# Performance work log

Measured on AMD Instinct MI355X. Metric: run time of the kernel, lower is better.

Reference implementation:

```python
import jax, jax.numpy as jnp
import numpy as np

B, S, T = 64, 1024, 64
H, A, DA, DT, P, NT = 1024, 1024, 512, 256, 256, 32
DIN = DA + A + DT  # LSTMCell input: [a_tm1_embed, att_tm1, pre_type]


def setup_inputs() -> dict:
    key = jax.random.key(0)
    ks = jax.random.split(key, 16)
    nrm = lambda k, shape, s=0.02: jax.random.normal(k, shape, jnp.float32) * s
    return {
        'src_encodings': jax.random.normal(ks[0], (B, S, H), jnp.float32),
        'W_ih': nrm(ks[1], (4 * H, DIN)), 'b_ih': jnp.zeros((4 * H,), jnp.float32),
        'W_hh': nrm(ks[2], (4 * H, H)), 'b_hh': jnp.zeros((4 * H,), jnp.float32),
        'W_att': nrm(ks[3], (H, H)),            # att_sketch_linear (no bias)
        'W_attvec': nrm(ks[4], (A, 2 * H)),     # sketch_att_vec_linear (no bias)
        'W_init': nrm(ks[5], (H, H)), 'b_init': jnp.zeros((H,), jnp.float32),  # decoder_cell_init
        'W_q2a': nrm(ks[6], (DA, A)), 'b_q2a': jnp.zeros((DA,), jnp.float32),  # query_vec_to_action_embed
        'prod_embed': nrm(ks[7], (P, DA), 0.05), 'prod_bias': jnp.zeros((P,), jnp.float32),
        'type_embed': nrm(ks[8], (NT, DT), 0.05),
        'prev_prod_ids': jax.random.randint(ks[9], (B, T), 0, P),
        'prev_type_ids': jax.random.randint(ks[10], (B, T), 0, NT),
        'target_prod_ids': jax.random.randint(ks[11], (B, T), 0, P),
        'sketch_lens': jax.random.randint(ks[12], (B,), T // 2, T + 1),
        'src_lens': jax.random.randint(ks[13], (B,), S // 2, S + 1),
    }


def _lstm_cell(x, h, c, W_ih, b_ih, W_hh, b_hh):
    gates = x @ W_ih.T + b_ih + h @ W_hh.T + b_hh
    i, f, g, o = jnp.split(gates, 4, axis=-1)
    c_new = jax.nn.sigmoid(f) * c + jax.nn.sigmoid(i) * jnp.tanh(g)
    h_new = jax.nn.sigmoid(o) * jnp.tanh(c_new)
    return h_new, c_new


def reference(src_encodings, W_ih, b_ih, W_hh, b_hh, W_att, W_attvec, W_init, b_init,
              W_q2a, b_q2a, prod_embed, prod_bias, type_embed,
              prev_prod_ids, prev_type_ids, target_prod_ids, sketch_lens, src_lens):
    Bq, Sq, Hq = src_encodings.shape
    Tq = prev_prod_ids.shape[1]
    src_valid = jnp.arange(Sq)[None, :] < src_lens[:, None]            # [B,S] True = real token
    step_valid = jnp.arange(Tq)[None, :] < sketch_lens[:, None]        # [B,T]
    prev_valid = step_valid & (jnp.arange(Tq)[None, :] > 0)            # prev action exists

    src_att = jnp.einsum('bsh,kh->bsk', src_encodings, W_att)          # att_sketch_linear
    # init_decoder_state(adaptive_avg_pool1d(enc,1))
    init_cell = src_encodings.mean(axis=1)
    h0 = jnp.tanh(init_cell @ W_init.T + b_init)
    c0 = jnp.zeros_like(h0)
    att0 = jnp.zeros((Bq, A), src_encodings.dtype)

    # precomputed grammar lookups (production / type embeddings of a_{t-1})
    a_embeds = jnp.where(prev_valid[..., None], prod_embed[prev_prod_ids], 0.0)   # [B,T,DA]
    t_embeds = jnp.where(prev_valid[..., None], type_embed[prev_type_ids], 0.0)   # [B,T,DT]
    is_first = jnp.arange(Tq) == 0                                                # [T]

    def step(carry, inp):
        h, c, att_tm1 = carry
        a_e, t_e, first = inp
        x = jnp.concatenate([a_e, att_tm1, t_e], axis=-1)
        x = jnp.where(first, 0.0, x)                                   # t==0 -> zero input
        h, c = _lstm_cell(x, h, c, W_ih, b_ih, W_hh, b_hh)
        scores = jnp.einsum('bh,bsh->bs', h, src_att)
        scores = jnp.where(src_valid, scores, -1e9)
        alpha = jax.nn.softmax(scores, axis=-1)
        ctx = jnp.einsum('bs,bsh->bh', alpha, src_encodings)
        att_t = jnp.tanh(jnp.concatenate([h, ctx], axis=-1) @ W_attvec.T)
        q = jnp.tanh(att_t @ W_q2a.T + b_q2a)                          # non_linear readout
        probs = jax.nn.softmax(q @ prod_embed.T + prod_bias, axis=-1)  # [B,P]
        return (h, c, att_t), probs

    xs = (jnp.swapaxes(a_embeds, 0, 1), jnp.swapaxes(t_embeds, 0, 1), is_first)
    _, probs = jax.lax.scan(step, (h0, c0, att0), xs)                  # [T,B,P]

    tgt = jnp.swapaxes(target_prod_ids, 0, 1)[..., None]               # [T,B,1]
    p_t = jnp.take_along_axis(probs, tgt, axis=-1)[..., 0]             # [T,B]
    logp = jnp.log(p_t + 1e-8)
    sketch_prob = jnp.sum(jnp.where(step_valid.T, logp, 0.0), axis=0)  # [B]
    return sketch_prob
```

## Files before the change

### kernel.cpp

```cpp
#include <hip/hip_runtime.h>
#include <hip/hip_bf16.h>

typedef unsigned short u16;
typedef unsigned char u8;
typedef unsigned int u32;
typedef unsigned long long u64;
typedef __attribute__((ext_vector_type(8))) short short8;
typedef __attribute__((ext_vector_type(8))) u16 ushort8;
typedef __attribute__((ext_vector_type(4))) float f32x4;
typedef __attribute__((ext_vector_type(2))) float f32x2;

__device__ __forceinline__ float bf2f(u16 x){ u32 u=((u32)x)<<16; return __builtin_bit_cast(float,u); }
__device__ __forceinline__ u16 f2bf(float f){ u32 u=__builtin_bit_cast(u32,f); u32 r=(u+0x7fffu+((u>>16)&1u))>>16; return (u16)r; }
__device__ __forceinline__ float sigf(float x){ return 1.f/(1.f+__expf(-x)); }

__device__ __forceinline__ void scf(float* p, float v){
  __hip_atomic_store(p, v, __ATOMIC_RELAXED, __HIP_MEMORY_SCOPE_AGENT);
}
__device__ __forceinline__ void scu16(u16* p, u16 v){
  __hip_atomic_store(p, v, __ATOMIC_RELAXED, __HIP_MEMORY_SCOPE_AGENT);
}


__global__ __launch_bounds__(256) void k_cast(const float* __restrict__ s, u16* __restrict__ d, long n){
  long i = ((long)blockIdx.x*256 + threadIdx.x)*8;
  if (i >= n) return;
  float4 a = *(const float4*)(s+i);
  float4 b = *(const float4*)(s+i+4);
  ushort8 o;
  o[0]=f2bf(a.x); o[1]=f2bf(a.y); o[2]=f2bf(a.z); o[3]=f2bf(a.w);
  o[4]=f2bf(b.x); o[5]=f2bf(b.y); o[6]=f2bf(b.z); o[7]=f2bf(b.w);
  *(ushort8*)(d+i) = o;
}

__global__ __launch_bounds__(256) void k_cast8(const float* __restrict__ s, u8* __restrict__ d, long n){
  long i = ((long)blockIdx.x*256 + threadIdx.x)*8;
  if (i >= n) return;
  float4 a = *(const float4*)(s+i);
  float4 b = *(const float4*)(s+i+4);
  u32 w0 = 0, w1 = 0;
  w0 = __builtin_amdgcn_cvt_pk_fp8_f32(a.x, a.y, w0, false);
  w0 = __builtin_amdgcn_cvt_pk_fp8_f32(a.z, a.w, w0, true);
  w1 = __builtin_amdgcn_cvt_pk_fp8_f32(b.x, b.y, w1, false);
  w1 = __builtin_amdgcn_cvt_pk_fp8_f32(b.z, b.w, w1, true);
  uint2 o; o.x = w0; o.y = w1;
  *(uint2*)(d+i) = o;
}

__global__ __launch_bounds__(256) void k_build_wc(const float* __restrict__ Wih, const float* __restrict__ Whh,
                                                  u16* __restrict__ WC){
  long i8 = (long)blockIdx.x*256 + threadIdx.x;
  if (i8 >= (long)4096*352) return;
  int j = (int)(i8/352); int kk = (int)(i8%352)*8;
  const float* src;
  if (kk < 512)        src = Wih + (long)j*1792 + kk;
  else if (kk < 768)   src = Wih + (long)j*1792 + (kk+1024);
  else if (kk < 1792)  src = Wih + (long)j*1792 + (kk-256);
  else                 src = Whh + (long)j*1024 + (kk-1792);
  u16* dst = WC + (long)j*2816 + kk;
  ushort8 o;
  #pragma unroll
  for (int q=0;q<8;++q) o[q] = f2bf(src[q]);
  *(ushort8*)dst = o;
}

__global__ __launch_bounds__(256) void k_wattT(const float* __restrict__ Wa, u16* __restrict__ WT){
  int id = blockIdx.x*256 + threadIdx.x;
  int m = id >> 10, k = id & 1023;
  WT[(long)m*1024 + k] = f2bf(Wa[(long)k*1024 + m]);
}

__global__ __launch_bounds__(256) void k_meanf(const float* __restrict__ enc, u16* __restrict__ MEANB){
  int b = blockIdx.x, h = blockIdx.y*256 + threadIdx.x;
  const float* p = enc + ((long)b<<20) + h;
  float s = 0.f;
  for (int ss=0; ss<1024; ++ss) s += p[(long)ss<<10];
  MEANB[b*1024 + h] = f2bf(s * (1.f/1024.f));
}

__global__ __launch_bounds__(256) void k_embed(const float* __restrict__ pemb, const float* __restrict__ temb,
      const int* __restrict__ pid, const int* __restrict__ tid_, const int* __restrict__ slen,
      u16* __restrict__ XC){
  int t = blockIdx.x >> 6, b = blockIdx.x & 63;
  bool valid = (t>0) && (t < slen[b]);
  int pi = pid[b*64 + t], ti = tid_[b*64 + t];
  u16* dst = XC + (long)blockIdx.x*2816;
  for (int kk = threadIdx.x; kk < 768; kk += 256){
    float v = 0.f;
    if (valid) v = (kk<512) ? pemb[(long)pi*512 + kk] : temb[(long)ti*256 + (kk-512)];
    dst[kk] = f2bf(v);
  }
}

__global__ void k_assign(const int* __restrict__ slen, int* __restrict__ ASG){
  if (threadIdx.x != 0 || blockIdx.x != 0) return;
  int lenv[64]; long total = 0;
  for (int b=0;b<64;++b){ int L = slen[b]; if (L<1)L=1; if (L>1024)L=1024; lenv[b]=L; total+=L; }
  int cnt[64]; int sum=0;
  for (int b=0;b<64;++b){
    int c = (int)(((long)256*lenv[b])/total);
    if (c<1)c=1; if (c>8)c=8; cnt[b]=c; sum+=c;
  }
  int rem = 256 - sum; int bi = 0;
  while (rem > 0){ if (cnt[bi&63] < 8){ cnt[bi&63]++; rem--; } bi++; }
  while (rem < 0){ if (cnt[bi&63] > 1){ cnt[bi&63]--; rem++; } bi++; }
  int st = 0;
  for (int b=0;b<64;++b){
    ASG[1024+b] = cnt[b];
    ASG[1088+b] = st;
    for (int i=0;i<cnt[b];++i){ ASG[st+i] = b; ASG[256+st+i] = i; }
    st += cnt[b];
  }
}

template<int MODE>
__global__ __launch_bounds__(256) void k_gemm(const u16* __restrict__ A, long lda,
      const u16* __restrict__ W, int K, const float* __restrict__ bias,
      float* __restrict__ OF, long ldo, u16* __restrict__ OB1, long ldb1){
  int l = threadIdx.x & 63, w = threadIdx.x >> 6;
  int c = l & 15, g = l >> 4;
  int n0 = blockIdx.x*16, m0 = blockIdx.y*64;
  const u16* ap = A + (long)(m0 + w*16 + c)*lda + g*8;
  const u16* bp = W + (long)(n0 + c)*K + g*8;
  f32x4 acc = {0.f,0.f,0.f,0.f};
  int kit = K >> 5;
  #pragma unroll 4
  for (int kb=0; kb<kit; ++kb){
    short8 av = *(const short8*)(ap + kb*32);
    short8 bv = *(const short8*)(bp + kb*32);
    acc = __builtin_amdgcn_mfma_f32_16x16x32_bf16(av, bv, acc, 0, 0, 0);
  }
  #pragma unroll
  for (int r=0;r<4;++r){
    int row = m0 + w*16 + g*4 + r;
    int col = n0 + c;
    float v = acc[r];
    if (MODE==2){ OB1[(long)row*ldb1 + col] = f2bf(tanhf(v + bias[col])); }
    if (MODE==3){ OF[(long)row*ldo + col] = v + bias[col]; }
  }
}

__global__ __launch_bounds__(256) void k_loss(const float* __restrict__ LG, const int* __restrict__ tgt,
      const int* __restrict__ slen, float* __restrict__ out){
  int b = blockIdx.x;
  int w = threadIdx.x >> 6, l = threadIdx.x & 63;
  int len = slen[b];
  float accum = 0.f;
  for (int t = w; t < 64; t += 4){
    if (t >= len) continue;
    const float* lp = LG + ((long)(t*64 + b))*256;
    float v0=lp[l], v1=lp[l+64], v2=lp[l+128], v3=lp[l+192];
    float mx = fmaxf(fmaxf(v0,v1), fmaxf(v2,v3));
    #pragma unroll
    for (int off=32; off; off>>=1) mx = fmaxf(mx, __shfl_xor(mx, off));
    float s = __expf(v0-mx)+__expf(v1-mx)+__expf(v2-mx)+__expf(v3-mx);
    #pragma unroll
    for (int off=32; off; off>>=1) s += __shfl_xor(s, off);
    float ltg = lp[tgt[b*64 + t]];
    float p = __expf(ltg - mx)/s;
    accum += logf(p + 1e-8f);
  }
  __shared__ float sm[4];
  if (l == 0) sm[w] = accum;
  __syncthreads();
  if (threadIdx.x == 0) out[b] = sm[0]+sm[1]+sm[2]+sm[3];
}

__device__ __forceinline__ void gsync(int* __restrict__ bar, int& gen){
  gen += 1;
  __syncthreads();
  if (threadIdx.x == 0){
    int grp = blockIdx.x & 15;
    int prev = __hip_atomic_fetch_add(bar + grp*64, 1, __ATOMIC_RELAXED, __HIP_MEMORY_SCOPE_AGENT);
    if (prev == gen*16 - 1)
      __hip_atomic_fetch_add(bar + 1024, 1, __ATOMIC_RELAXED, __HIP_MEMORY_SCOPE_AGENT);
    while (__hip_atomic_load(bar + 1024, __ATOMIC_RELAXED, __HIP_MEMORY_SCOPE_AGENT) < gen*16)
      __builtin_amdgcn_s_sleep(1);
  }
  __syncthreads();
}

__global__ __launch_bounds__(1024,1) void k_decoder(
      const u8* __restrict__ ENC8, const u16* __restrict__ WC,
      const u16* __restrict__ WAVT, const u16* __restrict__ WAVEC,
      const float* __restrict__ bih, const float* __restrict__ bhh,
      u16* __restrict__ XC, u16* __restrict__ ATT,
      float* __restrict__ HWT, float* __restrict__ PLT,
      u16* __restrict__ CTXBT, const int* __restrict__ src_lens,
      const int* __restrict__ ASG, int* __restrict__ BAR){
  const int tid = threadIdx.x;
  const int w = tid >> 6, l = tid & 63, c = l & 15, g = l >> 4;
  const int bx = blockIdx.x;
  int gen = 0;

  __shared__ float smem[12320];
  f32x4* lacc  = (f32x4*)smem;
  float* s_ctx = smem;
  float* s_ls  = smem + 12288;
  u16*   ldsc  = (u16*)smem;
  f32x4* lacc4 = (f32x4*)(smem + 8192);

  const int n0 = bx << 2;
  const int jrow = n0 + (c & 3) + ((c >> 2) << 10);
  const float biasj = bih[jrow] + bhh[jrow];
  const int kh = w >> 2, mt = w & 3;
  const int lbase = l & 0x33;
  float creg[4] = {0.f,0.f,0.f,0.f};
  const int mt2 = bx & 3, nt2 = bx >> 2;
  const int b3 = ASG[bx];
  const int ci3 = ASG[256 + bx];
  const int nch3 = ASG[1024 + b3];
  int len3 = src_lens[b3]; if (len3 < 1) len3 = 1; if (len3 > 1024) len3 = 1024;
  const int chunk3 = (len3 + nch3 - 1)/nch3;
  int s0 = ci3*chunk3;
  int s1 = s0 + chunk3; if (s1 > len3) s1 = len3; if (s0 > s1) s0 = s1;
  const u8* encb = ENC8 + (((long)b3)<<20);
  const int base = s0 + 2*w;
  const int mt4 = bx & 3, nt4 = bx >> 2;
  const int b16 = tid >> 6, lane64 = tid & 63;

  uint4 pa0,pa1, pb0,pb1;
  {
    int rA0 = (base   < s1) ? base   : s0;
    int rA1 = (base+1 < s1) ? base+1 : s0;
    pa0 = *(const uint4*)(encb + ((long)rA0<<10) + l*16);
    pa1 = *(const uint4*)(encb + ((long)rA1<<10) + l*16);
    int sB = base+32;
    int rB0 = (sB   < s1) ? sB   : s0;
    int rB1 = (sB+1 < s1) ? sB+1 : s0;
    pb0 = *(const uint4*)(encb + ((long)rB0<<10) + l*16);
    pb1 = *(const uint4*)(encb + ((long)rB1<<10) + l*16);
  }

  for (int t = 0; t < 64; ++t){
    const u16* XCt = XC + (size_t)t*64*2816;
    u16* XCn = XC + (size_t)(t+1)*64*2816;
    const u16* Hcur = XCn + 1792;
    float* HW   = HWT  + ((size_t)t<<16);
    float* PL   = PLT  + ((size_t)t<<8);
    u16*  CTXB  = CTXBT + ((size_t)t<<18);

    {
      const u16* ap = XCt + (long)(mt*16 + c)*2816 + kh*704 + g*8;
      const u16* bp = WC  + (long)jrow*2816 + kh*704 + g*8;
      f32x4 acc = {0.f,0.f,0.f,0.f};
      #pragma unroll 11
      for (int kb=0; kb<22; ++kb){
        short8 av = *(const short8*)(ap + kb*32);
        short8 bv = *(const short8*)(bp + kb*32);
        acc = __builtin_amdgcn_mfma_f32_16x16x32_bf16(av, bv, acc, 0, 0, 0);
      }
      lacc[w*64 + l] = acc;
      __syncthreads();
      if (w < 4){
        f32x4 a0 = lacc[w*64 + l];
        f32x4 a1 = lacc[(w+4)*64 + l];
        f32x4 a2 = lacc[(w+8)*64 + l];
        f32x4 a3 = lacc[(w+12)*64 + l];
        #pragma unroll
        for (int r=0;r<4;++r){
          float val = a0[r] + a1[r] + a2[r] + a3[r] + biasj;
          float iv = __shfl(val, lbase);
          float fv = __shfl(val, lbase+4);
          float gv = __shfl(val, lbase+8);
          float ov = __shfl(val, lbase+12);
          if ((l & 12) == 0){
            float cn = sigf(fv)*creg[r] + sigf(iv)*tanhf(gv);
            float hn = sigf(ov)*tanhf(cn);
            creg[r] = cn;
            int b = w*16 + g*4 + r;
            int n = n0 + (l & 3);
            scu16(XCn + (long)b*2816 + 1792 + n, f2bf(hn));
          }
        }
      }
    }
    gsync(BAR, gen);

    {
      const u16* ap = Hcur + (long)(mt2*16 + c)*2816 + w*64 + g*8;
      const u16* bp = WAVT + (long)(nt2*16 + c)*1024 + w*64 + g*8;
      f32x4 acc = {0.f,0.f,0.f,0.f};
      #pragma unroll
      for (int kb=0; kb<2; ++kb){
        short8 av = *(const short8*)(ap + kb*32);
        short8 bv = *(const short8*)(bp + kb*32);
        acc = __builtin_amdgcn_mfma_f32_16x16x32_bf16(av, bv, acc, 0, 0, 0);
      }
      lacc[w*64 + l] = acc;
      __syncthreads();
      if (w == 0){
        f32x4 rd = lacc[l];
        #pragma unroll
        for (int w2=1; w2<16; ++w2) rd += lacc[w2*64 + l];
        #pragma unroll
        for (int r=0;r<4;++r)
          scf(HW + (long)(mt2*16 + g*4 + r)*1024 + nt2*16 + c, rd[r]);
      }
    }
    gsync(BAR, gen);

    {
      float hw[16], ctx[16];
      const float* hwp = HW + b3*1024 + l*16;
      #pragma unroll
      for (int jj=0;jj<4;++jj){
        float4 v = *(const float4*)(hwp + jj*4);
        hw[4*jj]=v.x; hw[4*jj+1]=v.y; hw[4*jj+2]=v.z; hw[4*jj+3]=v.w;
      }
      #pragma unroll
      for (int jj=0;jj<16;++jj) ctx[jj]=0.f;
      float lsum = 0.f;
      for (int s = base; s < s1; s += 32){
        int sC = s + 64;
        int rC0 = (sC   < s1) ? sC   : s0;
        int rC1 = (sC+1 < s1) ? sC+1 : s0;
        uint4 pc0 = *(const uint4*)(encb + ((long)rC0<<10) + l*16);
        uint4 pc1 = *(const uint4*)(encb + ((long)rC1<<10) + l*16);
        float eA[16], eB[16];
        #pragma unroll
        for (int jj=0;jj<4;++jj){
          u32 xA = ((const u32*)&pa0)[jj];
          u32 xB = ((const u32*)&pa1)[jj];
          f32x2 la = __builtin_amdgcn_cvt_pk_f32_fp8(xA, false);
          f32x2 ha = __builtin_amdgcn_cvt_pk_f32_fp8(xA, true);
          f32x2 lb = __builtin_amdgcn_cvt_pk_f32_fp8(xB, false);
          f32x2 hb = __builtin_amdgcn_cvt_pk_f32_fp8(xB, true);
          eA[4*jj]=la[0]; eA[4*jj+1]=la[1]; eA[4*jj+2]=ha[0]; eA[4*jj+3]=ha[1];
          eB[4*jj]=lb[0]; eB[4*jj+1]=lb[1]; eB[4*jj+2]=hb[0]; eB[4*jj+3]=hb[1];
        }
        float scA = 0.f, scB = 0.f;
        #pragma unroll
        for (int jj=0;jj<16;++jj){ scA += eA[jj]*hw[jj]; scB += eB[jj]*hw[jj]; }
        #pragma unroll
        for (int off=32; off; off>>=1){
          scA += __shfl_xor(scA, off);
          scB += __shfl_xor(scB, off);
        }
        if (s+1 >= s1) scB = -1e30f;
        float peA = __expf(scA);
        float peB = __expf(scB);
        lsum += peA + peB;
        #pragma unroll
        for (int jj=0;jj<16;++jj) ctx[jj] += peA*eA[jj] + peB*eB[jj];
        pa0=pb0; pa1=pb1;
        pb0=pc0; pb1=pc1;
      }
      {
        int rA0 = (base   < s1) ? base   : s0;
        int rA1 = (base+1 < s1) ? base+1 : s0;
        pa0 = *(const uint4*)(encb + ((long)rA0<<10) + l*16);
        pa1 = *(const uint4*)(encb + ((long)rA1<<10) + l*16);
        int sB = base+32;
        int rB0 = (sB   < s1) ? sB   : s0;
        int rB1 = (sB+1 < s1) ? sB+1 : s0;
        pb0 = *(const uint4*)(encb + ((long)rB0<<10) + l*16);
        pb1 = *(const uint4*)(encb + ((long)rB1<<10) + l*16);
      }
      if (l == 0) s_ls[w] = lsum;
      if (w < 8){
        #pragma unroll
        for (int jj=0;jj<16;++jj) s_ctx[w*1024 + l*16 + jj] = ctx[jj];
      }
      __syncthreads();
      if (w >= 8){
        #pragma unroll
        for (int jj=0;jj<16;++jj) s_ctx[(w-8)*1024 + l*16 + jj] += ctx[jj];
      }
      __syncthreads();
      {
        float v = 0.f;
        #pragma unroll
        for (int p=0;p<8;++p) v += s_ctx[p*1024 + tid];
        scu16(CTXB + (((long)bx)<<10) + tid, f2bf(v));
      }
      if (tid == 0){
        float L = 0.f;
        #pragma unroll
        for (int q=0;q<16;++q) L += s_ls[q];
        scf(PL + bx, L);
      }
    }
    gsync(BAR, gen);

    {
      int b = mt4*16 + b16;
      int st = ASG[1088 + b], nL = ASG[1024 + b];
      float plv[8];
      #pragma unroll
      for (int p=0;p<8;++p){ int ip = st + ((p<nL)? p:0); plv[p] = PL[ip]; }
      float L = 0.f;
      #pragma unroll
      for (int p=0;p<8;++p) if (p<nL) L += plv[p];
      float inv = (L > 0.f) ? 1.f/L : 0.f;
      float acc16[16];
      #pragma unroll
      for (int q=0;q<16;++q) acc16[q] = 0.f;
      #pragma unroll
      for (int rnd=0; rnd<2; ++rnd){
        ushort8 va[4][2];
        #pragma unroll
        for (int q4=0;q4<4;++q4){
          int p = rnd*4+q4; int ip = st + ((p<nL)? p:0);
          const u16* row = CTXB + (((long)ip)<<10);
          va[q4][0] = *(const ushort8*)(row + lane64*8);
          va[q4][1] = *(const ushort8*)(row + (lane64+64)*8);
        }
        #pragma unroll
        for (int q4=0;q4<4;++q4){
          int p = rnd*4+q4;
          if (p<nL){
            #pragma unroll
            for (int j=0;j<8;++j){
              acc16[j]   += bf2f(va[q4][0][j]);
              acc16[8+j] += bf2f(va[q4][1][j]);
            }
          }
        }
      }
      const int swz = (b16 & 7) << 3;
      #pragma unroll
      for (int q=0;q<2;++q){
        int mcol8 = (lane64 + q*64)*8;
        ushort8 o;
        #pragma unroll
        for (int j=0;j<8;++j) o[j] = f2bf(acc16[q*8+j]*inv);
        *(ushort8*)(ldsc + ((b16*1024 + mcol8) ^ swz)) = o;
      }
      __syncthreads();
      f32x4 acc = {0.f,0.f,0.f,0.f};
      const int koff = (w < 8) ? w*128 : 1024 + (w-8)*128;
      const u16* bp = WAVEC + (long)(nt4*16 + c)*2048 + koff + g*8;
      if (w < 8){
        const u16* ap = Hcur + (long)(mt4*16 + c)*2816 + w*128 + g*8;
        #pragma unroll
        for (int kb=0; kb<4; ++kb){
          short8 av = *(const short8*)(ap + kb*32);
          short8 bv = *(const short8*)(bp + kb*32);
          acc = __builtin_amdgcn_mfma_f32_16x16x32_bf16(av, bv, acc, 0, 0, 0);
        }
      } else {
        const int cswz = (c & 7) << 3;
        const int kbase = c*1024 + (w-8)*128 + g*8;
        #pragma unroll
        for (int kb=0; kb<4; ++kb){
          short8 av = *(const short8*)(ldsc + ((kbase + kb*32) ^ cswz));
          short8 bv = *(const short8*)(bp + kb*32);
          acc = __builtin_amdgcn_mfma_f32_16x16x32_bf16(av, bv, acc, 0, 0, 0);
        }
      }
      lacc4[w*64 + l] = acc;
      __syncthreads();
      if (w == 0){
        f32x4 rd = lacc4[l];
        #pragma unroll
        for (int w2=1; w2<16; ++w2) rd += lacc4[w2*64 + l];
        #pragma unroll
        for (int r=0;r<4;++r){
          int b_ = mt4*16 + g*4 + r;
          int col = nt4*16 + c;
          u16 x = f2bf(tanhf(rd[r]));
          scu16(XCn + (long)b_*2816 + 768 + col, x);
          ATT[((long)t*64 + b_)*1024 + col] = x;
        }
      }
    }
    gsync(BAR, gen);
  }
}

extern "C" void kernel_launch(void* const* d_in, const int* in_sizes, int n_in,
                              void* d_out, int out_size, void* d_ws, size_t ws_size,
                              hipStream_t stream){
  const float* enc      = (const float*)d_in[0];
  const float* W_ih     = (const float*)d_in[1];
  const float* b_ih     = (const float*)d_in[2];
  const float* W_hh     = (const float*)d_in[3];
  const float* b_hh     = (const float*)d_in[4];
  const float* W_att    = (const float*)d_in[5];
  const float* W_attvec = (const float*)d_in[6];
  const float* W_init   = (const float*)d_in[7];
  const float* b_init   = (const float*)d_in[8];
  const float* W_q2a    = (const float*)d_in[9];
  const float* b_q2a    = (const float*)d_in[10];
  const float* prod_emb = (const float*)d_in[11];
  const float* prod_bias= (const float*)d_in[12];
  const float* type_emb = (const float*)d_in[13];
  const int* prev_pid   = (const int*)d_in[14];
  const int* prev_tid   = (const int*)d_in[15];
  const int* target     = (const int*)d_in[16];
  const int* sk_lens    = (const int*)d_in[17];
  const int* src_lens   = (const int*)d_in[18];
  float* out = (float*)d_out;

  char* ws = (char*)d_ws;
  size_t o = 0;
  auto alloc = [&](size_t bytes)->char*{ char* p = ws + o; o += (bytes + 255) & ~(size_t)255; return p; };
  u8*   ENC8 = (u8*)alloc((size_t)64*1024*1024);
  u16*  WC   = (u16*)alloc((size_t)4096*2816*2);
  u16*  WAVT = (u16*)alloc((size_t)1024*1024*2);
  u16*  WAVEC= (u16*)alloc((size_t)1024*2048*2);
  u16*  WQ   = (u16*)alloc((size_t)512*1024*2);
  u16*  PE   = (u16*)alloc((size_t)256*512*2);
  u16*  WINIT= (u16*)alloc((size_t)1024*1024*2);
  u16*  MEANB= (u16*)alloc((size_t)64*1024*2);
  u16*  XC   = (u16*)alloc((size_t)65*64*2816*2);
  u16*  ATT  = (u16*)alloc((size_t)64*64*1024*2);
  float* HWT = (float*)alloc((size_t)64*64*1024*4);
  float* PLT = (float*)alloc((size_t)64*256*4);
  u16*  CTXBT=(u16*)alloc((size_t)64*256*1024*2);
  u16*  Q    = (u16*)alloc((size_t)4096*512*2);
  float* LG  = (float*)alloc((size_t)4096*256*4);
  int*  BAR  = (int*)alloc(8192);
  int*  ASG  = (int*)alloc(8192);
  (void)ws_size; (void)in_sizes; (void)n_in; (void)out_size;

  hipMemsetAsync(XC, 0, (size_t)64*2816*2, stream);
  hipMemsetAsync(BAR, 0, 8192, stream);

  k_assign<<<1,64,0,stream>>>(src_lens, ASG);
  k_cast8<<<32768,256,0,stream>>>(enc, ENC8, (long)64*1024*1024);
  k_cast<<<1024,256,0,stream>>>(W_attvec, WAVEC, (long)1024*2048);
  k_cast<<<256,256,0,stream>>>(W_q2a, WQ, (long)512*1024);
  k_cast<<<64,256,0,stream>>>(prod_emb, PE, (long)256*512);
  k_cast<<<512,256,0,stream>>>(W_init, WINIT, (long)1024*1024);
  k_build_wc<<<5632,256,0,stream>>>(W_ih, W_hh, WC);
  k_wattT<<<4096,256,0,stream>>>(W_att, WAVT);
  k_meanf<<<dim3(64,4),256,0,stream>>>(enc, MEANB);
  k_gemm<2><<<dim3(64,1),256,0,stream>>>(MEANB, 1024L, WINIT, 1024, b_init,
                                         nullptr, 0L, XC + 1792, 2816L);
  k_embed<<<4096,256,0,stream>>>(prod_emb, type_emb, prev_pid, prev_tid, sk_lens, XC);

  k_decoder<<<256,1024,0,stream>>>(ENC8, WC, WAVT, WAVEC, b_ih, b_hh,
                                   XC, ATT, HWT, PLT, CTXBT, src_lens, ASG, BAR);

  k_gemm<2><<<dim3(32,64),256,0,stream>>>(ATT, 1024L, WQ, 1024, b_q2a,
                                          nullptr, 0L, Q, 512L);
  k_gemm<3><<<dim3(16,64),256,0,stream>>>(Q, 512L, PE, 512, prod_bias,
                                          LG, 256L, nullptr, 0L);
  k_loss<<<64,256,0,stream>>>(LG, target, sk_lens, out);
}
```

Before: 4.290 ms.

## Split grid barrier into arrive/wait and overlap independent GEMM work

The grid barrier is split into separate arrive and wait halves. Work that does not depend on the barrier is moved between the two so it overlaps the wait. The LSTM gate GEMM's contributions from the action/type embeddings and the hidden state of step t+1 are computed early, during the phase-2 barrier, leaving only the att_tm1 slice for phase 1. The h-half of the attention-vector GEMM is likewise computed before the phase-4 barrier completes. This hides barrier latency behind useful MFMA work, but relies on those inputs already being final when read early, which adds a subtle ordering risk.

```diff
diff --git a/kernel.cpp b/kernel.cpp
--- a/kernel.cpp
+++ b/kernel.cpp
@@ -166,18 +166,15 @@
   if (threadIdx.x == 0) out[b] = sm[0]+sm[1]+sm[2]+sm[3];
 }
 
-__device__ __forceinline__ void gsync(int* __restrict__ bar, int& gen){
-  gen += 1;
-  __syncthreads();
-  if (threadIdx.x == 0){
-    int grp = blockIdx.x & 15;
-    int prev = __hip_atomic_fetch_add(bar + grp*64, 1, __ATOMIC_RELAXED, __HIP_MEMORY_SCOPE_AGENT);
-    if (prev == gen*16 - 1)
-      __hip_atomic_fetch_add(bar + 1024, 1, __ATOMIC_RELAXED, __HIP_MEMORY_SCOPE_AGENT);
-    while (__hip_atomic_load(bar + 1024, __ATOMIC_RELAXED, __HIP_MEMORY_SCOPE_AGENT) < gen*16)
-      __builtin_amdgcn_s_sleep(1);
-  }
-  __syncthreads();
+__device__ __forceinline__ void barrier_arrive(int* __restrict__ bar, int gen1){
+  int grp = blockIdx.x & 15;
+  int prev = __hip_atomic_fetch_add(bar + grp*64, 1, __ATOMIC_RELAXED, __HIP_MEMORY_SCOPE_AGENT);
+  if (prev == gen1*16 - 1)
+    __hip_atomic_fetch_add(bar + 1024, 1, __ATOMIC_RELAXED, __HIP_MEMORY_SCOPE_AGENT);
+}
+__device__ __forceinline__ void barrier_wait(int* __restrict__ bar, int gen1){
+  while (__hip_atomic_load(bar + 1024, __ATOMIC_RELAXED, __HIP_MEMORY_SCOPE_AGENT) < gen1*16)
+    __builtin_amdgcn_s_sleep(1);
 }
 
 __global__ __launch_bounds__(1024,1) void k_decoder(
@@ -219,6 +216,27 @@
   const int mt4 = bx & 3, nt4 = bx >> 2;
   const int b16 = tid >> 6, lane64 = tid & 63;
 
+  f32x4 accA = {0.f,0.f,0.f,0.f};
+  auto run_p1a = [&](int tn, f32x4& aA){
+    const u16* xrow = XC + (size_t)tn*64*2816 + (long)(mt*16 + c)*2816;
+    const u16* wrow = WC + (long)jrow*2816;
+    #pragma unroll
+    for (int kb=0; kb<6; ++kb){
+      int col = kh*192 + kb*32 + g*8;
+      short8 av = *(const short8*)(xrow + col);
+      short8 bv = *(const short8*)(wrow + col);
+      aA = __builtin_amdgcn_mfma_f32_16x16x32_bf16(av, bv, aA, 0, 0, 0);
+    }
+    #pragma unroll
+    for (int kb=0; kb<8; ++kb){
+      int col = 1792 + kh*256 + kb*32 + g*8;
+      short8 av = *(const short8*)(xrow + col);
+      short8 bv = *(const short8*)(wrow + col);
+      aA = __builtin_amdgcn_mfma_f32_16x16x32_bf16(av, bv, aA, 0, 0, 0);
+    }
+  };
+  run_p1a(0, accA);
+
   uint4 pa0,pa1, pb0,pb1;
   {
     int rA0 = (base   < s1) ? base   : s0;
@@ -241,13 +259,14 @@
     u16*  CTXB  = CTXBT + ((size_t)t<<18);
 
     {
-      const u16* ap = XCt + (long)(mt*16 + c)*2816 + kh*704 + g*8;
-      const u16* bp = WC  + (long)jrow*2816 + kh*704 + g*8;
-      f32x4 acc = {0.f,0.f,0.f,0.f};
-      #pragma unroll 11
-      for (int kb=0; kb<22; ++kb){
-        short8 av = *(const short8*)(ap + kb*32);
-        short8 bv = *(const short8*)(bp + kb*32);
+      const u16* xrow = XCt + (long)(mt*16 + c)*2816;
+      const u16* wrow = WC + (long)jrow*2816;
+      f32x4 acc = accA;
+      #pragma unroll
+      for (int kb=0; kb<8; ++kb){
+        int col = 768 + kh*256 + kb*32 + g*8;
+        short8 av = *(const short8*)(xrow + col);
+        short8 bv = *(const short8*)(wrow + col);
         acc = __builtin_amdgcn_mfma_f32_16x16x32_bf16(av, bv, acc, 0, 0, 0);
       }
       lacc[w*64 + l] = acc;
@@ -275,7 +294,10 @@
         }
       }
     }
-    gsync(BAR, gen);
+    __syncthreads();
+    if (tid == 0) barrier_arrive(BAR, gen+1);
+    if (tid == 0) barrier_wait(BAR, gen+1);
+    gen++; __syncthreads();
 
     {
       const u16* ap = Hcur + (long)(mt2*16 + c)*2816 + w*64 + g*8;
@@ -298,7 +320,12 @@
           scf(HW + (long)(mt2*16 + g*4 + r)*1024 + nt2*16 + c, rd[r]);
       }
     }
-    gsync(BAR, gen);
+    __syncthreads();
+    if (tid == 0) barrier_arrive(BAR, gen+1);
+    accA = (f32x4){0.f,0.f,0.f,0.f};
+    run_p1a(t+1, accA);
+    if (tid == 0) barrier_wait(BAR, gen+1);
+    gen++; __syncthreads();
 
     {
       float hw[16], ctx[16];
@@ -381,7 +408,21 @@
         scf(PL + bx, L);
       }
     }
-    gsync(BAR, gen);
+    __syncthreads();
+    if (tid == 0) barrier_arrive(BAR, gen+1);
+    f32x4 accP4 = {0.f,0.f,0.f,0.f};
+    {
+      const u16* aph = Hcur + (long)(mt4*16 + c)*2816 + w*64 + g*8;
+      const u16* bph = WAVEC + (long)(nt4*16 + c)*2048 + w*64 + g*8;
+      #pragma unroll
+      for (int kb=0; kb<2; ++kb){
+        short8 av = *(const short8*)(aph + kb*32);
+        short8 bv = *(const short8*)(bph + kb*32);
+        accP4 = __builtin_amdgcn_mfma_f32_16x16x32_bf16(av, bv, accP4, 0, 0, 0);
+      }
+    }
+    if (tid == 0) barrier_wait(BAR, gen+1);
+    gen++; __syncthreads();
 
     {
       int b = mt4*16 + b16;
@@ -428,28 +469,16 @@
         *(ushort8*)(ldsc + ((b16*1024 + mcol8) ^ swz)) = o;
       }
       __syncthreads();
-      f32x4 acc = {0.f,0.f,0.f,0.f};
-      const int koff = (w < 8) ? w*128 : 1024 + (w-8)*128;
-      const u16* bp = WAVEC + (long)(nt4*16 + c)*2048 + koff + g*8;
-      if (w < 8){
-        const u16* ap = Hcur + (long)(mt4*16 + c)*2816 + w*128 + g*8;
-        #pragma unroll
-        for (int kb=0; kb<4; ++kb){
-          short8 av = *(const short8*)(ap + kb*32);
-          short8 bv = *(const short8*)(bp + kb*32);
-          acc = __builtin_amdgcn_mfma_f32_16x16x32_bf16(av, bv, acc, 0, 0, 0);
-        }
-      } else {
-        const int cswz = (c & 7) << 3;
-        const int kbase = c*1024 + (w-8)*128 + g*8;
-        #pragma unroll
-        for (int kb=0; kb<4; ++kb){
-          short8 av = *(const short8*)(ldsc + ((kbase + kb*32) ^ cswz));
-          short8 bv = *(const short8*)(bp + kb*32);
-          acc = __builtin_amdgcn_mfma_f32_16x16x32_bf16(av, bv, acc, 0, 0, 0);
-        }
-      }
-      lacc4[w*64 + l] = acc;
+      const u16* bpc = WAVEC + (long)(nt4*16 + c)*2048 + 1024 + w*64 + g*8;
+      const int cswz = (c & 7) << 3;
+      const int kbase = c*1024 + w*64 + g*8;
+      #pragma unroll
+      for (int kb=0; kb<2; ++kb){
+        short8 av = *(const short8*)(ldsc + ((kbase + kb*32) ^ cswz));
+        short8 bv = *(const short8*)(bpc + kb*32);
+        accP4 = __builtin_amdgcn_mfma_f32_16x16x32_bf16(av, bv, accP4, 0, 0, 0);
+      }
+      lacc4[w*64 + l] = accP4;
       __syncthreads();
       if (w == 0){
         f32x4 rd = lacc4[l];
@@ -465,7 +494,10 @@
         }
       }
     }
-    gsync(BAR, gen);
+    __syncthreads();
+    if (tid == 0) barrier_arrive(BAR, gen+1);
+    if (tid == 0) barrier_wait(BAR, gen+1);
+    gen++; __syncthreads();
   }
 }
 
```

New measurement: 4.248 ms. About the same (-1.0%).

## Replace grid barriers with targeted flag waits and register-cache encoder rows

Applied to the files above, without the earlier changes.

Replaces the four global grid barriers per step with finer-grained flag counters. Blocks now wait only on the groups that produce the data they need, and a dedicated reduction stage combines the per-chunk context partials into a new buffer. The load-balanced batch-to-block assignment kernel is dropped in favour of a fixed 4 blocks per batch row. Each wave keeps up to 12 encoder rows in registers across all timesteps instead of reloading them every step. The aim is to cut barrier latency and repeated encoder reads, at the cost of more register pressure, possible load imbalance for uneven src lengths, and an extra serialized reduction stage on 64 blocks.

```diff
diff --git a/kernel.cpp b/kernel.cpp
--- a/kernel.cpp
+++ b/kernel.cpp
@@ -19,6 +19,12 @@
 }
 __device__ __forceinline__ void scu16(u16* p, u16 v){
   __hip_atomic_store(p, v, __ATOMIC_RELAXED, __HIP_MEMORY_SCOPE_AGENT);
+}
+__device__ __forceinline__ int ald(const int* p){
+  return __hip_atomic_load(p, __ATOMIC_RELAXED, __HIP_MEMORY_SCOPE_AGENT);
+}
+__device__ __forceinline__ void aadd(int* p){
+  __hip_atomic_fetch_add(p, 1, __ATOMIC_RELAXED, __HIP_MEMORY_SCOPE_AGENT);
 }
 
 
@@ -89,27 +95,6 @@
     float v = 0.f;
     if (valid) v = (kk<512) ? pemb[(long)pi*512 + kk] : temb[(long)ti*256 + (kk-512)];
     dst[kk] = f2bf(v);
-  }
-}
-
-__global__ void k_assign(const int* __restrict__ slen, int* __restrict__ ASG){
-  if (threadIdx.x != 0 || blockIdx.x != 0) return;
-  int lenv[64]; long total = 0;
-  for (int b=0;b<64;++b){ int L = slen[b]; if (L<1)L=1; if (L>1024)L=1024; lenv[b]=L; total+=L; }
-  int cnt[64]; int sum=0;
-  for (int b=0;b<64;++b){
-    int c = (int)(((long)256*lenv[b])/total);
-    if (c<1)c=1; if (c>8)c=8; cnt[b]=c; sum+=c;
-  }
-  int rem = 256 - sum; int bi = 0;
-  while (rem > 0){ if (cnt[bi&63] < 8){ cnt[bi&63]++; rem--; } bi++; }
-  while (rem < 0){ if (cnt[bi&63] > 1){ cnt[bi&63]--; rem++; } bi++; }
-  int st = 0;
-  for (int b=0;b<64;++b){
-    ASG[1024+b] = cnt[b];
-    ASG[1088+b] = st;
-    for (int i=0;i<cnt[b];++i){ ASG[st+i] = b; ASG[256+st+i] = i; }
-    st += cnt[b];
   }
 }
 
@@ -166,19 +151,6 @@
   if (threadIdx.x == 0) out[b] = sm[0]+sm[1]+sm[2]+sm[3];
 }
 
-__device__ __forceinline__ void gsync(int* __restrict__ bar, int& gen){
-  gen += 1;
-  __syncthreads();
-  if (threadIdx.x == 0){
-    int grp = blockIdx.x & 15;
-    int prev = __hip_atomic_fetch_add(bar + grp*64, 1, __ATOMIC_RELAXED, __HIP_MEMORY_SCOPE_AGENT);
-    if (prev == gen*16 - 1)
-      __hip_atomic_fetch_add(bar + 1024, 1, __ATOMIC_RELAXED, __HIP_MEMORY_SCOPE_AGENT);
-    while (__hip_atomic_load(bar + 1024, __ATOMIC_RELAXED, __HIP_MEMORY_SCOPE_AGENT) < gen*16)
-      __builtin_amdgcn_s_sleep(1);
-  }
-  __syncthreads();
-}
 
 __global__ __launch_bounds__(1024,1) void k_decoder(
       const u8* __restrict__ ENC8, const u16* __restrict__ WC,
@@ -186,12 +158,11 @@
       const float* __restrict__ bih, const float* __restrict__ bhh,
       u16* __restrict__ XC, u16* __restrict__ ATT,
       float* __restrict__ HWT, float* __restrict__ PLT,
-      u16* __restrict__ CTXBT, const int* __restrict__ src_lens,
-      const int* __restrict__ ASG, int* __restrict__ BAR){
+      u16* __restrict__ CTXBT, u16* __restrict__ CTXFT,
+      const int* __restrict__ src_lens, int* __restrict__ BAR){
   const int tid = threadIdx.x;
   const int w = tid >> 6, l = tid & 63, c = l & 15, g = l >> 4;
   const int bx = blockIdx.x;
-  int gen = 0;
 
   __shared__ float smem[12320];
   f32x4* lacc  = (f32x4*)smem;
@@ -199,6 +170,12 @@
   float* s_ls  = smem + 12288;
   u16*   ldsc  = (u16*)smem;
   f32x4* lacc4 = (f32x4*)(smem + 8192);
+
+  int* F1  = BAR;
+  int* F4  = BAR + 256;
+  int* F2  = BAR + 512;
+  int* F3  = BAR + 576;
+  int* F3c = BAR + 640;
 
   const int n0 = bx << 2;
   const int jrow = n0 + (c & 3) + ((c >> 2) << 10);
@@ -207,38 +184,35 @@
   const int lbase = l & 0x33;
   float creg[4] = {0.f,0.f,0.f,0.f};
   const int mt2 = bx & 3, nt2 = bx >> 2;
-  const int b3 = ASG[bx];
-  const int ci3 = ASG[256 + bx];
-  const int nch3 = ASG[1024 + b3];
+  const int b3 = bx >> 2, ci3 = bx & 3;
   int len3 = src_lens[b3]; if (len3 < 1) len3 = 1; if (len3 > 1024) len3 = 1024;
-  const int chunk3 = (len3 + nch3 - 1)/nch3;
+  const int chunk3 = (len3 + 3) >> 2;
   int s0 = ci3*chunk3;
-  int s1 = s0 + chunk3; if (s1 > len3) s1 = len3; if (s0 > s1) s0 = s1;
+  int s1 = s0 + chunk3; if (s1 > len3) s1 = len3;
   const u8* encb = ENC8 + (((long)b3)<<20);
-  const int base = s0 + 2*w;
+  int lim = s1 - s0 - w;
+  int nqv = (lim <= 0) ? 0 : ((lim + 15) >> 4);
+  if (nqv > 16) nqv = 16;
   const int mt4 = bx & 3, nt4 = bx >> 2;
-  const int b16 = tid >> 6, lane64 = tid & 63;
-
-  uint4 pa0,pa1, pb0,pb1;
-  {
-    int rA0 = (base   < s1) ? base   : s0;
-    int rA1 = (base+1 < s1) ? base+1 : s0;
-    pa0 = *(const uint4*)(encb + ((long)rA0<<10) + l*16);
-    pa1 = *(const uint4*)(encb + ((long)rA1<<10) + l*16);
-    int sB = base+32;
-    int rB0 = (sB   < s1) ? sB   : s0;
-    int rB1 = (sB+1 < s1) ? sB+1 : s0;
-    pb0 = *(const uint4*)(encb + ((long)rB0<<10) + l*16);
-    pb1 = *(const uint4*)(encb + ((long)rB1<<10) + l*16);
+  const int grp = bx & 15;
+
+  uint4 er[12];
+  #pragma unroll
+  for (int q=0;q<12;++q){
+    int r = s0 + q*16 + w;
+    if (r >= s1) r = s0;
+    er[q] = *(const uint4*)(encb + ((long)r<<10) + l*16);
   }
 
   for (int t = 0; t < 64; ++t){
+    const int gen = t + 1;
     const u16* XCt = XC + (size_t)t*64*2816;
     u16* XCn = XC + (size_t)(t+1)*64*2816;
     const u16* Hcur = XCn + 1792;
     float* HW   = HWT  + ((size_t)t<<16);
     float* PL   = PLT  + ((size_t)t<<8);
     u16*  CTXB  = CTXBT + ((size_t)t<<18);
+    u16*  CTXF  = CTXFT + ((size_t)t<<16);
 
     {
       const u16* ap = XCt + (long)(mt*16 + c)*2816 + kh*704 + g*8;
@@ -275,7 +249,18 @@
         }
       }
     }
-    gsync(BAR, gen);
+    __syncthreads();
+    if (tid == 0) aadd(F1 + grp*16);
+    if (tid < 64){
+      const int* pf = F1 + (tid & 15)*16;
+      int tgt = gen*16;
+      for(;;){
+        int v = ald(pf);
+        if (__all(v >= tgt)) break;
+        __builtin_amdgcn_s_sleep(1);
+      }
+    }
+    __syncthreads();
 
     {
       const u16* ap = Hcur + (long)(mt2*16 + c)*2816 + w*64 + g*8;
@@ -298,7 +283,12 @@
           scf(HW + (long)(mt2*16 + g*4 + r)*1024 + nt2*16 + c, rd[r]);
       }
     }
-    gsync(BAR, gen);
+    __syncthreads();
+    if (tid == 0){
+      aadd(F2 + mt2*16);
+      while (ald(F2 + (bx>>6)*16) < gen*64) __builtin_amdgcn_s_sleep(1);
+    }
+    __syncthreads();
 
     {
       float hw[16], ctx[16];
@@ -311,51 +301,30 @@
       #pragma unroll
       for (int jj=0;jj<16;++jj) ctx[jj]=0.f;
       float lsum = 0.f;
-      for (int s = base; s < s1; s += 32){
-        int sC = s + 64;
-        int rC0 = (sC   < s1) ? sC   : s0;
-        int rC1 = (sC+1 < s1) ? sC+1 : s0;
-        uint4 pc0 = *(const uint4*)(encb + ((long)rC0<<10) + l*16);
-        uint4 pc1 = *(const uint4*)(encb + ((long)rC1<<10) + l*16);
-        float eA[16], eB[16];
+      auto proc = [&](uint4 ev){
+        float e[16];
         #pragma unroll
         for (int jj=0;jj<4;++jj){
-          u32 xA = ((const u32*)&pa0)[jj];
-          u32 xB = ((const u32*)&pa1)[jj];
-          f32x2 la = __builtin_amdgcn_cvt_pk_f32_fp8(xA, false);
-          f32x2 ha = __builtin_amdgcn_cvt_pk_f32_fp8(xA, true);
-          f32x2 lb = __builtin_amdgcn_cvt_pk_f32_fp8(xB, false);
-          f32x2 hb = __builtin_amdgcn_cvt_pk_f32_fp8(xB, true);
-          eA[4*jj]=la[0]; eA[4*jj+1]=la[1]; eA[4*jj+2]=ha[0]; eA[4*jj+3]=ha[1];
-          eB[4*jj]=lb[0]; eB[4*jj+1]=lb[1]; eB[4*jj+2]=hb[0]; eB[4*jj+3]=hb[1];
+          u32 x = ((const u32*)&ev)[jj];
+          f32x2 lo = __builtin_amdgcn_cvt_pk_f32_fp8(x, false);
+          f32x2 hi = __builtin_amdgcn_cvt_pk_f32_fp8(x, true);
+          e[4*jj]=lo[0]; e[4*jj+1]=lo[1]; e[4*jj+2]=hi[0]; e[4*jj+3]=hi[1];
         }
-        float scA = 0.f, scB = 0.f;
-        #pragma unroll
-        for (int jj=0;jj<16;++jj){ scA += eA[jj]*hw[jj]; scB += eB[jj]*hw[jj]; }
-        #pragma unroll
-        for (int off=32; off; off>>=1){
-          scA += __shfl_xor(scA, off);
-          scB += __shfl_xor(scB, off);
-        }
-        if (s+1 >= s1) scB = -1e30f;
-        float peA = __expf(scA);
-        float peB = __expf(scB);
-        lsum += peA + peB;
-        #pragma unroll
-        for (int jj=0;jj<16;++jj) ctx[jj] += peA*eA[jj] + peB*eB[jj];
-        pa0=pb0; pa1=pb1;
-        pb0=pc0; pb1=pc1;
-      }
-      {
-        int rA0 = (base   < s1) ? base   : s0;
-        int rA1 = (base+1 < s1) ? base+1 : s0;
-        pa0 = *(const uint4*)(encb + ((long)rA0<<10) + l*16);
-        pa1 = *(const uint4*)(encb + ((long)rA1<<10) + l*16);
-        int sB = base+32;
-        int rB0 = (sB   < s1) ? sB   : s0;
-        int rB1 = (sB+1 < s1) ? sB+1 : s0;
-        pb0 = *(const uint4*)(encb + ((long)rB0<<10) + l*16);
-        pb1 = *(const uint4*)(encb + ((long)rB1<<10) + l*16);
+        float sc = 0.f;
+        #pragma unroll
+        for (int jj=0;jj<16;++jj) sc += e[jj]*hw[jj];
+        #pragma unroll
+        for (int off=32; off; off>>=1) sc += __shfl_xor(sc, off);
+        float pe = __expf(sc);
+        lsum += pe;
+        #pragma unroll
+        for (int jj=0;jj<16;++jj) ctx[jj] += pe*e[jj];
+      };
+      #pragma unroll
+      for (int q=0;q<12;++q) if (q < nqv) proc(er[q]);
+      for (int q=12; q<nqv; ++q){
+        uint4 ev = *(const uint4*)(encb + ((long)(s0 + q*16 + w)<<10) + l*16);
+        proc(ev);
       }
       if (l == 0) s_ls[w] = lsum;
       if (w < 8){
@@ -381,52 +350,39 @@
         scf(PL + bx, L);
       }
     }
-    gsync(BAR, gen);
+    __syncthreads();
+    if (tid == 0) aadd(F3 + (bx>>6)*16);
+
+    if (bx < 64){
+      if (tid == 0){
+        while (ald(F3 + (bx>>4)*16) < gen*64) __builtin_amdgcn_s_sleep(1);
+      }
+      __syncthreads();
+      int b = bx;
+      float L = PL[b*4] + PL[b*4+1] + PL[b*4+2] + PL[b*4+3];
+      float inv = (L > 0.f) ? 1.f/L : 0.f;
+      const u16* c0 = CTXB + (long)(b*4+0)*1024;
+      const u16* c1 = CTXB + (long)(b*4+1)*1024;
+      const u16* c2 = CTXB + (long)(b*4+2)*1024;
+      const u16* c3 = CTXB + (long)(b*4+3)*1024;
+      float v = bf2f(c0[tid]) + bf2f(c1[tid]) + bf2f(c2[tid]) + bf2f(c3[tid]);
+      scu16(CTXF + (long)b*1024 + tid, f2bf(v*inv));
+      __syncthreads();
+      if (tid == 0) aadd(F3c + (bx>>4)*16);
+    }
+    if (tid == 0){
+      while (ald(F3c + mt4*16) < gen*16) __builtin_amdgcn_s_sleep(1);
+    }
+    __syncthreads();
 
     {
-      int b = mt4*16 + b16;
-      int st = ASG[1088 + b], nL = ASG[1024 + b];
-      float plv[8];
-      #pragma unroll
-      for (int p=0;p<8;++p){ int ip = st + ((p<nL)? p:0); plv[p] = PL[ip]; }
-      float L = 0.f;
-      #pragma unroll
-      for (int p=0;p<8;++p) if (p<nL) L += plv[p];
-      float inv = (L > 0.f) ? 1.f/L : 0.f;
-      float acc16[16];
-      #pragma unroll
-      for (int q=0;q<16;++q) acc16[q] = 0.f;
-      #pragma unroll
-      for (int rnd=0; rnd<2; ++rnd){
-        ushort8 va[4][2];
-        #pragma unroll
-        for (int q4=0;q4<4;++q4){
-          int p = rnd*4+q4; int ip = st + ((p<nL)? p:0);
-          const u16* row = CTXB + (((long)ip)<<10);
-          va[q4][0] = *(const ushort8*)(row + lane64*8);
-          va[q4][1] = *(const ushort8*)(row + (lane64+64)*8);
-        }
-        #pragma unroll
-        for (int q4=0;q4<4;++q4){
-          int p = rnd*4+q4;
-          if (p<nL){
-            #pragma unroll
-            for (int j=0;j<8;++j){
-              acc16[j]   += bf2f(va[q4][0][j]);
-              acc16[8+j] += bf2f(va[q4][1][j]);
-            }
-          }
-        }
-      }
+      const int b16 = w;
+      const u16* cf = CTXF + (long)(mt4*16 + b16)*1024;
+      ushort8 v0 = *(const ushort8*)(cf + l*8);
+      ushort8 v1 = *(const ushort8*)(cf + (l+64)*8);
       const int swz = (b16 & 7) << 3;
-      #pragma unroll
-      for (int q=0;q<2;++q){
-        int mcol8 = (lane64 + q*64)*8;
-        ushort8 o;
-        #pragma unroll
-        for (int j=0;j<8;++j) o[j] = f2bf(acc16[q*8+j]*inv);
-        *(ushort8*)(ldsc + ((b16*1024 + mcol8) ^ swz)) = o;
-      }
+      *(ushort8*)(ldsc + ((b16*1024 + l*8) ^ swz)) = v0;
+      *(ushort8*)(ldsc + ((b16*1024 + (l+64)*8) ^ swz)) = v1;
       __syncthreads();
       f32x4 acc = {0.f,0.f,0.f,0.f};
       const int koff = (w < 8) ? w*128 : 1024 + (w-8)*128;
@@ -465,7 +421,18 @@
         }
       }
     }
-    gsync(BAR, gen);
+    __syncthreads();
+    if (tid == 0) aadd(F4 + grp*16);
+    if (tid < 64){
+      const int* pf = F4 + (tid & 15)*16;
+      int tgt = gen*16;
+      for(;;){
+        int v = ald(pf);
+        if (__all(v >= tgt)) break;
+        __builtin_amdgcn_s_sleep(1);
+      }
+    }
+    __syncthreads();
   }
 }
 
@@ -509,16 +476,15 @@
   float* HWT = (float*)alloc((size_t)64*64*1024*4);
   float* PLT = (float*)alloc((size_t)64*256*4);
   u16*  CTXBT=(u16*)alloc((size_t)64*256*1024*2);
+  u16*  CTXFT=(u16*)alloc((size_t)64*64*1024*2);
   u16*  Q    = (u16*)alloc((size_t)4096*512*2);
   float* LG  = (float*)alloc((size_t)4096*256*4);
-  int*  BAR  = (int*)alloc(8192);
-  int*  ASG  = (int*)alloc(8192);
+  int*  BAR  = (int*)alloc(4096);
   (void)ws_size; (void)in_sizes; (void)n_in; (void)out_size;
 
   hipMemsetAsync(XC, 0, (size_t)64*2816*2, stream);
-  hipMemsetAsync(BAR, 0, 8192, stream);
-
-  k_assign<<<1,64,0,stream>>>(src_lens, ASG);
+  hipMemsetAsync(BAR, 0, 4096, stream);
+
   k_cast8<<<32768,256,0,stream>>>(enc, ENC8, (long)64*1024*1024);
   k_cast<<<1024,256,0,stream>>>(W_attvec, WAVEC, (long)1024*2048);
   k_cast<<<256,256,0,stream>>>(W_q2a, WQ, (long)512*1024);
@@ -532,7 +498,7 @@
   k_embed<<<4096,256,0,stream>>>(prod_emb, type_emb, prev_pid, prev_tid, sk_lens, XC);
 
   k_decoder<<<256,1024,0,stream>>>(ENC8, WC, WAVT, WAVEC, b_ih, b_hh,
-                                   XC, ATT, HWT, PLT, CTXBT, src_lens, ASG, BAR);
+                                   XC, ATT, HWT, PLT, CTXBT, CTXFT, src_lens, BAR);
 
   k_gemm<2><<<dim3(32,64),256,0,stream>>>(ATT, 1024L, WQ, 1024, b_q2a,
                                           nullptr, 0L, Q, 512L);
```

Result: slower. 4.493 ms (+4.7%).
